# Kernel optimization log

Measured on AMD Instinct MI355X. Metric: run time of the kernel, lower is better.

The kernel has to match this reference:

```python
import jax, jax.numpy as jnp
import numpy as np

LN_EPS = 1e-6  # flax.linen.LayerNorm default


def setup_inputs() -> dict:
    key = jax.random.key(0)
    ks = jax.random.split(key, 16)
    N_TOT, M = 32768, 12            # total atoms, neighbors per atom
    ORIG, EDGE = 92, 41             # CGCNN atom / edge feature dims
    F, H, L = 128, 256, 3           # atom_fea_len, h_fea_len, n_conv

    def w(k, shape, fan_in):
        return jax.random.normal(k, shape, dtype=jnp.float32) / np.sqrt(fan_in).astype(np.float32)

    return {
        "atom_fea": jax.random.normal(ks[0], (N_TOT, ORIG), dtype=jnp.float32),
        "nbr_fea": jax.random.normal(ks[1], (N_TOT, M, EDGE), dtype=jnp.float32),
        "nbr_fea_idx": jax.random.randint(ks[2], (N_TOT, M), 0, N_TOT),
        # embedding Dense
        "W_embed": w(ks[3], (ORIG, F), ORIG), "b_embed": jnp.zeros((F,), jnp.float32),
        # per-conv-layer stacked params [L, ...]
        "W_center": w(ks[4], (L, F, F), F), "b_center": jnp.zeros((L, F), jnp.float32),
        "W_nbr": w(ks[5], (L, F, F), F), "b_nbr": jnp.zeros((L, F), jnp.float32),
        "W_edge": w(ks[6], (L, EDGE, F), EDGE), "b_edge": jnp.zeros((L, F), jnp.float32),
        "W_gate": w(ks[7], (L, F, F), F), "b_gate": jnp.zeros((L, F), jnp.float32),
        "W_mag": w(ks[8], (L, F, F), F), "b_mag": jnp.zeros((L, F), jnp.float32),
        "ln_scale": jnp.ones((L, F), jnp.float32), "ln_bias": jnp.zeros((L, F), jnp.float32),
        # readout: Dense(h) -> softplus -> Dense(1)
        "W_h": w(ks[9], (F, H), F), "b_h": jnp.zeros((H,), jnp.float32),
        "W_out": w(ks[10], (H, 1), H), "b_out": jnp.zeros((1,), jnp.float32),
        "batch_size": 128,
        "n_atoms_per_crystal": 256,
    }


def _layernorm(x, scale, bias):
    mu = jnp.mean(x, axis=-1, keepdims=True)
    var = jnp.mean(jnp.square(x - mu), axis=-1, keepdims=True)
    return (x - mu) * jax.lax.rsqrt(var + LN_EPS) * scale + bias


def reference(atom_fea, nbr_fea, nbr_fea_idx, W_embed, b_embed,
              W_center, b_center, W_nbr, b_nbr, W_edge, b_edge,
              W_gate, b_gate, W_mag, b_mag, ln_scale, ln_bias,
              W_h, b_h, W_out, b_out, batch_size, n_atoms_per_crystal):
    n_conv = W_center.shape[0]
    x = atom_fea @ W_embed + b_embed                       # [N, F]
    for i in range(n_conv):
        atom_nbr = jnp.take(x, nbr_fea_idx, axis=0)        # [N, M, F] gather
        # Dense on tiled center == Dense on center then broadcast
        phi_c = (x @ W_center[i] + b_center[i])[:, None, :]   # [N, 1, F]
        phi_n = atom_nbr @ W_nbr[i] + b_nbr[i]                # [N, M, F]
        phi_e = nbr_fea @ W_edge[i] + b_edge[i]               # [N, M, F]
        inter = phi_c * phi_n * phi_e                          # [N, M, F]
        gate = jax.nn.sigmoid(inter @ W_gate[i] + b_gate[i])
        mag = jax.nn.softplus(inter @ W_mag[i] + b_mag[i])
        nbr_sumed = jnp.sum(gate * mag, axis=1)               # [N, F]
        x = x + _layernorm(nbr_sumed, ln_scale[i], ln_bias[i])
    E_site = jax.nn.softplus(x @ W_h + b_h) @ W_out + b_out   # [N, 1]
    return jnp.sum(E_site.reshape(batch_size, n_atoms_per_crystal), axis=1, keepdims=True)  # [B, 1]
```

## Files before the change

kernel.cpp:

```cpp
#include <hip/hip_runtime.h>
#include <math.h>

#define N_TOT 32768
#define M_NBR 12
#define ORIG  92
#define EDGE  41
#define FD    128
#define HD    256
#define APC   256
#define NCRY  128

#define STR   136
#define WF_PER_LAYER 73728
#define WF_EMBED     12288
#define WF_H         32768

typedef __attribute__((ext_vector_type(8))) short bf16x8;
typedef __attribute__((ext_vector_type(4))) float f32x4;

__device__ __forceinline__ short f2bf(float f) {
    union { float f; unsigned u; } v; v.f = f;
    unsigned r = v.u + 0x7fffu + ((v.u >> 16) & 1u);
    return (short)(r >> 16);
}
__device__ __forceinline__ float bf2f(short s) {
    union { unsigned u; float f; } v; v.u = ((unsigned)(unsigned short)s) << 16;
    return v.f;
}
__device__ __forceinline__ float softplus_f(float x) {
    return fmaxf(x, 0.0f) + __logf(1.0f + __expf(-fabsf(x)));
}
__device__ __forceinline__ float sigmoid_f(float x) {
    return 1.0f / (1.0f + __expf(-x));
}

__global__ __launch_bounds__(256) void swizzle_kernel(
    const float* __restrict__ Wc_all, const float* __restrict__ Wn_all,
    const float* __restrict__ We_all, const float* __restrict__ Wg_all,
    const float* __restrict__ Wm_all, const float* __restrict__ W_embed,
    const float* __restrict__ W_h, short* __restrict__ dst_all)
{
    int gid = blockIdx.x * 256 + threadIdx.x;
    if (gid >= 33280) return;
    const float* W; short* dst; int K_real, fid, stride, l, nt, kt;
    if (gid < 27648) {
        int layer = gid / 9216;
        int rem = gid - layer * 9216;
        short* dbase = dst_all + layer * WF_PER_LAYER;
        if (rem < 2048)      { W = Wc_all + layer * 16384; dst = dbase;         K_real = 128; fid = rem; }
        else if (rem < 4096) { W = Wn_all + layer * 16384; dst = dbase + 16384; K_real = 128; fid = rem - 2048; }
        else if (rem < 5120) { W = We_all + layer * 5248;  dst = dbase + 32768; K_real = 41;  fid = rem - 4096; }
        else if (rem < 7168) { W = Wg_all + layer * 16384; dst = dbase + 40960; K_real = 128; fid = rem - 5120; }
        else                 { W = Wm_all + layer * 16384; dst = dbase + 57344; K_real = 128; fid = rem - 7168; }
        stride = 128; l = fid & 63; nt = (fid >> 6) & 7; kt = fid >> 9;
    } else if (gid < 29184) {
        fid = gid - 27648;
        W = W_embed; dst = dst_all + 3 * WF_PER_LAYER; K_real = ORIG; stride = 128;
        l = fid & 63; nt = (fid >> 6) & 7; kt = fid >> 9;
    } else {
        fid = gid - 29184;
        W = W_h; dst = dst_all + 3 * WF_PER_LAYER + WF_EMBED; K_real = 128; stride = 256;
        l = fid & 63; nt = (fid >> 6) & 15; kt = fid >> 10;
    }
    int n = nt * 16 + (l & 15), kb = kt * 32 + (l >> 4) * 8;
    bf16x8 v;
    #pragma unroll
    for (int j = 0; j < 8; ++j) {
        int k = kb + j;
        v[j] = (k < K_real) ? f2bf(W[k * stride + n]) : (short)0;
    }
    *(bf16x8*)(dst + fid * 8) = v;
}

__global__ __launch_bounds__(256) void embed_mfma_kernel(
    const float* __restrict__ atom_fea, const short* __restrict__ wef,
    const float* __restrict__ b, float* __restrict__ x, short* __restrict__ xbf)
{
    const int tid = threadIdx.x;
    const int w = tid >> 6, lane = tid & 63;
    const int q = lane >> 4, m = lane & 15;
    const int a0 = blockIdx.x * 64;
    const int arow = a0 + w * 16 + m;

    bf16x8 aA[3];
    const float* ap = atom_fea + (long)arow * ORIG;
    #pragma unroll
    for (int kt = 0; kt < 3; ++kt) {
        const int kb = kt * 32 + q * 8;
        bf16x8 v;
        if (kb + 7 < ORIG) {
            const float4 u0 = *(const float4*)(ap + kb);
            const float4 u1 = *(const float4*)(ap + kb + 4);
            v[0]=f2bf(u0.x); v[1]=f2bf(u0.y); v[2]=f2bf(u0.z); v[3]=f2bf(u0.w);
            v[4]=f2bf(u1.x); v[5]=f2bf(u1.y); v[6]=f2bf(u1.z); v[7]=f2bf(u1.w);
        } else {
            #pragma unroll
            for (int j = 0; j < 8; ++j) {
                const int k = kb + j;
                v[j] = (k < ORIG) ? f2bf(ap[k]) : (short)0;
            }
        }
        aA[kt] = v;
    }

    #pragma unroll
    for (int nt = 0; nt < 8; ++nt) {
        f32x4 C = {0.f, 0.f, 0.f, 0.f};
        #pragma unroll
        for (int kt = 0; kt < 3; ++kt)
            C = __builtin_amdgcn_mfma_f32_16x16x32_bf16(
                    aA[kt], *(const bf16x8*)(wef + ((kt * 8 + nt) * 64 + lane) * 8), C, 0, 0, 0);
        const int col = nt * 16 + m;
        const float bv = b[col];
        #pragma unroll
        for (int r = 0; r < 4; ++r) {
            const long n = a0 + w * 16 + q * 4 + r;
            const float val = C[r] + bv;
            x[n * FD + col] = val;
            xbf[n * FD + col] = f2bf(val);
        }
    }
}

__global__ __launch_bounds__(256) void conv_mfma_kernel(
    const float* __restrict__ x_in, const short* __restrict__ xbf_in,
    float* __restrict__ x_out, short* __restrict__ xbf_out,
    const float* __restrict__ nbr_fea, const int* __restrict__ nbr_idx,
    const short* __restrict__ wf,
    const float* __restrict__ bc, const float* __restrict__ bn,
    const float* __restrict__ be, const float* __restrict__ bg,
    const float* __restrict__ bm,
    const float* __restrict__ lns, const float* __restrict__ lnb)
{
    __shared__ short inter_s[192 * STR];
    __shared__ float phic_s[16 * 132];
    __shared__ int   idx_s[192];

    const int tid = threadIdx.x;
    const int w = tid >> 6, lane = tid & 63;
    const int q = lane >> 4, m = lane & 15;
    const int a0 = blockIdx.x * 16;
    const long r0 = (long)a0 * M_NBR;

    const short* Wc = wf;
    const short* Wn = wf + 16384;
    const short* We = wf + 32768;
    const short* Wg = wf + 40960;
    const short* Wm = wf + 57344;

    if (tid < 192) idx_s[tid] = nbr_idx[r0 + tid];

    {
        bf16x8 aC[4];
        #pragma unroll
        for (int kt = 0; kt < 4; ++kt)
            aC[kt] = *(const bf16x8*)(xbf_in + ((long)(a0 + m) << 7) + kt * 32 + q * 8);
        #pragma unroll
        for (int ii = 0; ii < 2; ++ii) {
            const int nt = w * 2 + ii;
            f32x4 C = {0.f, 0.f, 0.f, 0.f};
            #pragma unroll
            for (int kt = 0; kt < 4; ++kt)
                C = __builtin_amdgcn_mfma_f32_16x16x32_bf16(
                        aC[kt], *(const bf16x8*)(Wc + ((kt * 8 + nt) * 64 + lane) * 8), C, 0, 0, 0);
            const int col = nt * 16 + m;
            const float bcv = bc[col];
            #pragma unroll
            for (int r = 0; r < 4; ++r)
                phic_s[(q * 4 + r) * 132 + col] = C[r] + bcv;
        }
    }
    __syncthreads();

    bf16x8 aN[3][4];
    #pragma unroll
    for (int i = 0; i < 3; ++i) {
        const int row = (w * 3 + i) * 16 + m;
        const long g = (long)idx_s[row] << 7;
        #pragma unroll
        for (int kt = 0; kt < 4; ++kt)
            aN[i][kt] = *(const bf16x8*)(xbf_in + g + kt * 32 + q * 8);
    }
    bf16x8 aE[3][2];
    #pragma unroll
    for (int i = 0; i < 3; ++i) {
        const int row = (w * 3 + i) * 16 + m;
        const float* ep = nbr_fea + (r0 + row) * EDGE;
        bf16x8 e0, e1;
        #pragma unroll
        for (int j = 0; j < 8; ++j) e0[j] = f2bf(ep[q * 8 + j]);
        #pragma unroll
        for (int j = 0; j < 8; ++j) e1[j] = 0;
        if (q == 0) {
            #pragma unroll
            for (int j = 0; j < 8; ++j) e1[j] = f2bf(ep[32 + j]);
        } else if (q == 1) {
            e1[0] = f2bf(ep[40]);
        }
        aE[i][0] = e0; aE[i][1] = e1;
    }

    #pragma unroll
    for (int nt = 0; nt < 8; ++nt) {
        f32x4 Cn[3], Ce[3];
        #pragma unroll
        for (int i = 0; i < 3; ++i) { Cn[i] = (f32x4){0.f,0.f,0.f,0.f}; Ce[i] = (f32x4){0.f,0.f,0.f,0.f}; }
        #pragma unroll
        for (int kt = 0; kt < 4; ++kt) {
            const bf16x8 bfr = *(const bf16x8*)(Wn + ((kt * 8 + nt) * 64 + lane) * 8);
            #pragma unroll
            for (int i = 0; i < 3; ++i)
                Cn[i] = __builtin_amdgcn_mfma_f32_16x16x32_bf16(aN[i][kt], bfr, Cn[i], 0, 0, 0);
        }
        #pragma unroll
        for (int kt = 0; kt < 2; ++kt) {
            const bf16x8 efr = *(const bf16x8*)(We + ((kt * 8 + nt) * 64 + lane) * 8);
            #pragma unroll
            for (int i = 0; i < 3; ++i)
                Ce[i] = __builtin_amdgcn_mfma_f32_16x16x32_bf16(aE[i][kt], efr, Ce[i], 0, 0, 0);
        }
        const int col = nt * 16 + m;
        const float bnv = bn[col], bev = be[col];
        #pragma unroll
        for (int i = 0; i < 3; ++i) {
            const int rb = (w * 3 + i) * 16 + q * 4;
            #pragma unroll
            for (int r = 0; r < 4; ++r) {
                const int row = rb + r;
                const int atom = row / 12;
                const float iv = phic_s[atom * 132 + col] * (Cn[i][r] + bnv) * (Ce[i][r] + bev);
                inter_s[row * STR + col] = f2bf(iv);
            }
        }
    }

    bf16x8 aI[3][4];
    #pragma unroll
    for (int i = 0; i < 3; ++i) {
        const int row = (w * 3 + i) * 16 + m;
        #pragma unroll
        for (int kt = 0; kt < 4; ++kt)
            aI[i][kt] = *(const bf16x8*)(inter_s + row * STR + kt * 32 + q * 8);
    }

    #pragma unroll
    for (int nt = 0; nt < 8; ++nt) {
        f32x4 Cg[3], Cm[3];
        #pragma unroll
        for (int i = 0; i < 3; ++i) { Cg[i] = (f32x4){0.f,0.f,0.f,0.f}; Cm[i] = (f32x4){0.f,0.f,0.f,0.f}; }
        #pragma unroll
        for (int kt = 0; kt < 4; ++kt) {
            const bf16x8 gfr = *(const bf16x8*)(Wg + ((kt * 8 + nt) * 64 + lane) * 8);
            const bf16x8 mfr = *(const bf16x8*)(Wm + ((kt * 8 + nt) * 64 + lane) * 8);
            #pragma unroll
            for (int i = 0; i < 3; ++i) {
                Cg[i] = __builtin_amdgcn_mfma_f32_16x16x32_bf16(aI[i][kt], gfr, Cg[i], 0, 0, 0);
                Cm[i] = __builtin_amdgcn_mfma_f32_16x16x32_bf16(aI[i][kt], mfr, Cm[i], 0, 0, 0);
            }
        }
        const int col = nt * 16 + m;
        const float bgv = bg[col], bmv = bm[col];
        #pragma unroll
        for (int i = 0; i < 3; ++i) {
            const int rb = (w * 3 + i) * 16 + q * 4;
            #pragma unroll
            for (int r = 0; r < 4; ++r) {
                const float g = sigmoid_f(Cg[i][r] + bgv);
                const float s = softplus_f(Cm[i][r] + bmv);
                inter_s[(rb + r) * STR + col] = f2bf(g * s);
            }
        }
    }
    __syncthreads();

    {
        const int a = tid >> 4;
        const int cg = tid & 15;
        float s8[8];
        #pragma unroll
        for (int j = 0; j < 8; ++j) s8[j] = 0.f;
        #pragma unroll
        for (int nb = 0; nb < 12; ++nb) {
            const bf16x8 p = *(const bf16x8*)(inter_s + (a * 12 + nb) * STR + cg * 8);
            #pragma unroll
            for (int j = 0; j < 8; ++j) s8[j] += bf2f(p[j]);
        }
        float lsum = 0.f, lsq = 0.f;
        #pragma unroll
        for (int j = 0; j < 8; ++j) { lsum += s8[j]; lsq += s8[j] * s8[j]; }
        #pragma unroll
        for (int off = 1; off < 16; off <<= 1) {
            lsum += __shfl_xor(lsum, off, 64);
            lsq  += __shfl_xor(lsq,  off, 64);
        }
        const float mu = lsum * (1.0f / FD);
        float var = lsq * (1.0f / FD) - mu * mu;
        var = fmaxf(var, 0.0f);
        const float inv = rsqrtf(var + 1e-6f);
        const long xb = ((long)(a0 + a) << 7) + cg * 8;
        float o[8]; bf16x8 ob;
        #pragma unroll
        for (int j = 0; j < 8; ++j) {
            const int col = cg * 8 + j;
            const float y = (s8[j] - mu) * inv * lns[col] + lnb[col];
            const float v = x_in[xb + j] + y;
            o[j] = v; ob[j] = f2bf(v);
        }
        *(float4*)(x_out + xb)     = make_float4(o[0], o[1], o[2], o[3]);
        *(float4*)(x_out + xb + 4) = make_float4(o[4], o[5], o[6], o[7]);
        *(bf16x8*)(xbf_out + xb)   = ob;
    }
}

__global__ __launch_bounds__(256) void readout_mfma_kernel(
    const short* __restrict__ xbf, const short* __restrict__ whf,
    const float* __restrict__ bh, const float* __restrict__ Wo,
    const float* __restrict__ bo, float* __restrict__ out)
{
    const int tid = threadIdx.x;
    const int w = tid >> 6, lane = tid & 63;
    const int q = lane >> 4, m = lane & 15;
    const int a0 = blockIdx.x * 64;
    const int arow = a0 + w * 16 + m;

    bf16x8 aX[4];
    #pragma unroll
    for (int kt = 0; kt < 4; ++kt)
        aX[kt] = *(const bf16x8*)(xbf + ((long)arow << 7) + kt * 32 + q * 8);

    float e[4] = {0.f, 0.f, 0.f, 0.f};
    #pragma unroll
    for (int nt = 0; nt < 16; ++nt) {
        f32x4 C = {0.f, 0.f, 0.f, 0.f};
        #pragma unroll
        for (int kt = 0; kt < 4; ++kt)
            C = __builtin_amdgcn_mfma_f32_16x16x32_bf16(
                    aX[kt], *(const bf16x8*)(whf + ((kt * 16 + nt) * 64 + lane) * 8), C, 0, 0, 0);
        const int col = nt * 16 + m;
        const float bhv = bh[col], wov = Wo[col];
        #pragma unroll
        for (int r = 0; r < 4; ++r)
            e[r] += softplus_f(C[r] + bhv) * wov;
    }
    float esum = e[0] + e[1] + e[2] + e[3];
    #pragma unroll
    for (int off = 32; off > 0; off >>= 1)
        esum += __shfl_xor(esum, off, 64);
    if (lane == 0)
        atomicAdd(&out[a0 / APC], esum + 16.0f * bo[0]);
}

__global__ void zero_out_kernel(float* __restrict__ out) {
    if (threadIdx.x < NCRY) out[threadIdx.x] = 0.0f;
}

extern "C" void kernel_launch(void* const* d_in, const int* in_sizes, int n_in,
                              void* d_out, int out_size, void* d_ws, size_t ws_size,
                              hipStream_t stream) {
    const float* atom_fea = (const float*)d_in[0];
    const float* nbr_fea  = (const float*)d_in[1];
    const int*   nbr_idx  = (const int*)d_in[2];
    const float* W_embed  = (const float*)d_in[3];
    const float* b_embed  = (const float*)d_in[4];
    const float* W_center = (const float*)d_in[5];
    const float* b_center = (const float*)d_in[6];
    const float* W_nbr    = (const float*)d_in[7];
    const float* b_nbr    = (const float*)d_in[8];
    const float* W_edge   = (const float*)d_in[9];
    const float* b_edge   = (const float*)d_in[10];
    const float* W_gate   = (const float*)d_in[11];
    const float* b_gate   = (const float*)d_in[12];
    const float* W_mag    = (const float*)d_in[13];
    const float* b_mag    = (const float*)d_in[14];
    const float* ln_scale = (const float*)d_in[15];
    const float* ln_bias  = (const float*)d_in[16];
    const float* W_h      = (const float*)d_in[17];
    const float* b_h      = (const float*)d_in[18];
    const float* W_out    = (const float*)d_in[19];
    const float* b_out    = (const float*)d_in[20];

    float* out = (float*)d_out;
    const size_t NX = (size_t)N_TOT * FD;
    float* xA = (float*)d_ws;
    float* xB = xA + NX;
    short* xbfA = (short*)(xB + NX);
    short* xbfB = xbfA + NX;
    short* wfrag = xbfB + NX;

    swizzle_kernel<<<130, 256, 0, stream>>>(W_center, W_nbr, W_edge, W_gate, W_mag,
                                            W_embed, W_h, wfrag);
    embed_mfma_kernel<<<N_TOT / 64, 256, 0, stream>>>(
        atom_fea, wfrag + 3 * WF_PER_LAYER, b_embed, xA, xbfA);

    const float* xi = xA; float* xo = xB;
    const short* xbi = xbfA; short* xbo = xbfB;
    for (int l = 0; l < 3; ++l) {
        conv_mfma_kernel<<<N_TOT / 16, 256, 0, stream>>>(
            xi, xbi, xo, xbo, nbr_fea, nbr_idx,
            wfrag + (size_t)l * WF_PER_LAYER,
            b_center + (size_t)l * FD, b_nbr + (size_t)l * FD,
            b_edge + (size_t)l * FD, b_gate + (size_t)l * FD,
            b_mag + (size_t)l * FD,
            ln_scale + (size_t)l * FD, ln_bias + (size_t)l * FD);
        const float* tf = xo; xo = (float*)xi; xi = tf;
        const short* tb = xbo; xbo = (short*)xbi; xbi = tb;
    }

    zero_out_kernel<<<1, 128, 0, stream>>>(out);
    readout_mfma_kernel<<<N_TOT / 64, 256, 0, stream>>>(
        xbi, wfrag + 3 * WF_PER_LAYER + WF_EMBED, b_h, W_out, b_out, out);
}
```

Baseline: 469.3 us.

## Swap MFMA operands for row-contiguous outputs, use hardware bf16 pack and fast math

Swaps the A/B operands of the MFMA calls so each lane holds four consecutive output columns of one row. The epilogues can then use float4 bias loads and packed 64-bit stores to LDS and global memory instead of scalar strided stores. Replaces the software round-to-nearest bf16 conversion with the v_cvt_pk_bf16_f32 instruction, and uses rcp and log2 intrinsics in sigmoid and softplus to cut ALU work in the epilogues. LDS store patterns change, which may introduce bank conflicts, and the fast intrinsics slightly change numerics.

```diff
diff --git a/kernel.cpp b/kernel.cpp
--- a/kernel.cpp
+++ b/kernel.cpp
@@ -11,6 +11,7 @@
 #define NCRY  128
 
 #define STR   136
+#define PCS   132
 #define WF_PER_LAYER 73728
 #define WF_EMBED     12288
 #define WF_H         32768
@@ -18,20 +19,23 @@
 typedef __attribute__((ext_vector_type(8))) short bf16x8;
 typedef __attribute__((ext_vector_type(4))) float f32x4;
 
-__device__ __forceinline__ short f2bf(float f) {
-    union { float f; unsigned u; } v; v.f = f;
-    unsigned r = v.u + 0x7fffu + ((v.u >> 16) & 1u);
-    return (short)(r >> 16);
-}
+union BF8 { bf16x8 v; unsigned u[4]; };
+
+__device__ __forceinline__ unsigned pk2(float lo, float hi) {
+    unsigned r;
+    asm("v_cvt_pk_bf16_f32 %0, %1, %2" : "=v"(r) : "v"(lo), "v"(hi));
+    return r;
+}
+__device__ __forceinline__ short f2bf(float f) { return (short)pk2(f, f); }
 __device__ __forceinline__ float bf2f(short s) {
     union { unsigned u; float f; } v; v.u = ((unsigned)(unsigned short)s) << 16;
     return v.f;
 }
 __device__ __forceinline__ float softplus_f(float x) {
-    return fmaxf(x, 0.0f) + __logf(1.0f + __expf(-fabsf(x)));
+    return fmaxf(x, 0.0f) + 0.6931471805599453f * __log2f(1.0f + __expf(-fabsf(x)));
 }
 __device__ __forceinline__ float sigmoid_f(float x) {
-    return 1.0f / (1.0f + __expf(-x));
+    return __builtin_amdgcn_rcpf(1.0f + __expf(-x));
 }
 
 __global__ __launch_bounds__(256) void swizzle_kernel(
@@ -82,43 +86,37 @@
     const int a0 = blockIdx.x * 64;
     const int arow = a0 + w * 16 + m;
 
-    bf16x8 aA[3];
+    BF8 aA[3];
     const float* ap = atom_fea + (long)arow * ORIG;
     #pragma unroll
     for (int kt = 0; kt < 3; ++kt) {
         const int kb = kt * 32 + q * 8;
-        bf16x8 v;
+        BF8 t;
         if (kb + 7 < ORIG) {
             const float4 u0 = *(const float4*)(ap + kb);
             const float4 u1 = *(const float4*)(ap + kb + 4);
-            v[0]=f2bf(u0.x); v[1]=f2bf(u0.y); v[2]=f2bf(u0.z); v[3]=f2bf(u0.w);
-            v[4]=f2bf(u1.x); v[5]=f2bf(u1.y); v[6]=f2bf(u1.z); v[7]=f2bf(u1.w);
+            t.u[0] = pk2(u0.x, u0.y); t.u[1] = pk2(u0.z, u0.w);
+            t.u[2] = pk2(u1.x, u1.y); t.u[3] = pk2(u1.z, u1.w);
         } else {
-            #pragma unroll
-            for (int j = 0; j < 8; ++j) {
-                const int k = kb + j;
-                v[j] = (k < ORIG) ? f2bf(ap[k]) : (short)0;
-            }
-        }
-        aA[kt] = v;
-    }
-
-    #pragma unroll
-    for (int nt = 0; nt < 8; ++nt) {
+            const float4 u0 = *(const float4*)(ap + kb);
+            t.u[0] = pk2(u0.x, u0.y); t.u[1] = pk2(u0.z, u0.w);
+            t.u[2] = 0u; t.u[3] = 0u;
+        }
+        aA[kt] = t;
+    }
+
+    #pragma unroll
+    for (int ct = 0; ct < 8; ++ct) {
         f32x4 C = {0.f, 0.f, 0.f, 0.f};
         #pragma unroll
         for (int kt = 0; kt < 3; ++kt)
             C = __builtin_amdgcn_mfma_f32_16x16x32_bf16(
-                    aA[kt], *(const bf16x8*)(wef + ((kt * 8 + nt) * 64 + lane) * 8), C, 0, 0, 0);
-        const int col = nt * 16 + m;
-        const float bv = b[col];
-        #pragma unroll
-        for (int r = 0; r < 4; ++r) {
-            const long n = a0 + w * 16 + q * 4 + r;
-            const float val = C[r] + bv;
-            x[n * FD + col] = val;
-            xbf[n * FD + col] = f2bf(val);
-        }
+                    *(const bf16x8*)(wef + ((kt * 8 + ct) * 64 + lane) * 8), aA[kt].v, C, 0, 0, 0);
+        const float4 bv = *(const float4*)(b + ct * 16 + q * 4);
+        const float o0 = C[0] + bv.x, o1 = C[1] + bv.y, o2 = C[2] + bv.z, o3 = C[3] + bv.w;
+        const long base = ((long)arow << 7) + ct * 16 + q * 4;
+        *(float4*)(x + base) = make_float4(o0, o1, o2, o3);
+        *(uint2*)(xbf + base) = make_uint2(pk2(o0, o1), pk2(o2, o3));
     }
 }
 
@@ -133,7 +131,7 @@
     const float* __restrict__ lns, const float* __restrict__ lnb)
 {
     __shared__ short inter_s[192 * STR];
-    __shared__ float phic_s[16 * 132];
+    __shared__ float phic_s[16 * PCS];
     __shared__ int   idx_s[192];
 
     const int tid = threadIdx.x;
@@ -157,17 +155,15 @@
             aC[kt] = *(const bf16x8*)(xbf_in + ((long)(a0 + m) << 7) + kt * 32 + q * 8);
         #pragma unroll
         for (int ii = 0; ii < 2; ++ii) {
-            const int nt = w * 2 + ii;
+            const int ct = w * 2 + ii;
             f32x4 C = {0.f, 0.f, 0.f, 0.f};
             #pragma unroll
             for (int kt = 0; kt < 4; ++kt)
                 C = __builtin_amdgcn_mfma_f32_16x16x32_bf16(
-                        aC[kt], *(const bf16x8*)(Wc + ((kt * 8 + nt) * 64 + lane) * 8), C, 0, 0, 0);
-            const int col = nt * 16 + m;
-            const float bcv = bc[col];
-            #pragma unroll
-            for (int r = 0; r < 4; ++r)
-                phic_s[(q * 4 + r) * 132 + col] = C[r] + bcv;
+                        *(const bf16x8*)(Wc + ((kt * 8 + ct) * 64 + lane) * 8), aC[kt], C, 0, 0, 0);
+            const float4 bv = *(const float4*)(bc + ct * 16 + q * 4);
+            *(float4*)(phic_s + m * PCS + ct * 16 + q * 4) =
+                make_float4(C[0] + bv.x, C[1] + bv.y, C[2] + bv.z, C[3] + bv.w);
         }
     }
     __syncthreads();
@@ -186,51 +182,62 @@
     for (int i = 0; i < 3; ++i) {
         const int row = (w * 3 + i) * 16 + m;
         const float* ep = nbr_fea + (r0 + row) * EDGE;
-        bf16x8 e0, e1;
-        #pragma unroll
-        for (int j = 0; j < 8; ++j) e0[j] = f2bf(ep[q * 8 + j]);
-        #pragma unroll
-        for (int j = 0; j < 8; ++j) e1[j] = 0;
+        BF8 e0, e1;
+        const int kb = q * 8;
+        e0.u[0] = pk2(ep[kb + 0], ep[kb + 1]);
+        e0.u[1] = pk2(ep[kb + 2], ep[kb + 3]);
+        e0.u[2] = pk2(ep[kb + 4], ep[kb + 5]);
+        e0.u[3] = pk2(ep[kb + 6], ep[kb + 7]);
+        e1.u[0] = 0u; e1.u[1] = 0u; e1.u[2] = 0u; e1.u[3] = 0u;
         if (q == 0) {
-            #pragma unroll
-            for (int j = 0; j < 8; ++j) e1[j] = f2bf(ep[32 + j]);
+            e1.u[0] = pk2(ep[32], ep[33]);
+            e1.u[1] = pk2(ep[34], ep[35]);
+            e1.u[2] = pk2(ep[36], ep[37]);
+            e1.u[3] = pk2(ep[38], ep[39]);
         } else if (q == 1) {
-            e1[0] = f2bf(ep[40]);
-        }
-        aE[i][0] = e0; aE[i][1] = e1;
-    }
-
-    #pragma unroll
-    for (int nt = 0; nt < 8; ++nt) {
+            e1.u[0] = pk2(ep[40], 0.0f);
+        }
+        aE[i][0] = e0.v; aE[i][1] = e1.v;
+    }
+
+    int atomL[3];
+    #pragma unroll
+    for (int i = 0; i < 3; ++i)
+        atomL[i] = (w * 48 + i * 16 + m) / 12;
+
+    #pragma unroll
+    for (int ct = 0; ct < 8; ++ct) {
         f32x4 Cn[3], Ce[3];
         #pragma unroll
-        for (int i = 0; i < 3; ++i) { Cn[i] = (f32x4){0.f,0.f,0.f,0.f}; Ce[i] = (f32x4){0.f,0.f,0.f,0.f}; }
+        for (int i = 0; i < 3; ++i) {
+            Cn[i] = (f32x4){0.f, 0.f, 0.f, 0.f};
+            Ce[i] = (f32x4){0.f, 0.f, 0.f, 0.f};
+        }
         #pragma unroll
         for (int kt = 0; kt < 4; ++kt) {
-            const bf16x8 bfr = *(const bf16x8*)(Wn + ((kt * 8 + nt) * 64 + lane) * 8);
+            const bf16x8 nfr = *(const bf16x8*)(Wn + ((kt * 8 + ct) * 64 + lane) * 8);
             #pragma unroll
             for (int i = 0; i < 3; ++i)
-                Cn[i] = __builtin_amdgcn_mfma_f32_16x16x32_bf16(aN[i][kt], bfr, Cn[i], 0, 0, 0);
+                Cn[i] = __builtin_amdgcn_mfma_f32_16x16x32_bf16(nfr, aN[i][kt], Cn[i], 0, 0, 0);
         }
         #pragma unroll
         for (int kt = 0; kt < 2; ++kt) {
-            const bf16x8 efr = *(const bf16x8*)(We + ((kt * 8 + nt) * 64 + lane) * 8);
+            const bf16x8 efr = *(const bf16x8*)(We + ((kt * 8 + ct) * 64 + lane) * 8);
             #pragma unroll
             for (int i = 0; i < 3; ++i)
-                Ce[i] = __builtin_amdgcn_mfma_f32_16x16x32_bf16(aE[i][kt], efr, Ce[i], 0, 0, 0);
-        }
-        const int col = nt * 16 + m;
-        const float bnv = bn[col], bev = be[col];
+                Ce[i] = __builtin_amdgcn_mfma_f32_16x16x32_bf16(efr, aE[i][kt], Ce[i], 0, 0, 0);
+        }
+        const float4 bnv = *(const float4*)(bn + ct * 16 + q * 4);
+        const float4 bev = *(const float4*)(be + ct * 16 + q * 4);
         #pragma unroll
         for (int i = 0; i < 3; ++i) {
-            const int rb = (w * 3 + i) * 16 + q * 4;
-            #pragma unroll
-            for (int r = 0; r < 4; ++r) {
-                const int row = rb + r;
-                const int atom = row / 12;
-                const float iv = phic_s[atom * 132 + col] * (Cn[i][r] + bnv) * (Ce[i][r] + bev);
-                inter_s[row * STR + col] = f2bf(iv);
-            }
+            const float4 pc = *(const float4*)(phic_s + atomL[i] * PCS + ct * 16 + q * 4);
+            const float v0 = pc.x * (Cn[i][0] + bnv.x) * (Ce[i][0] + bev.x);
+            const float v1 = pc.y * (Cn[i][1] + bnv.y) * (Ce[i][1] + bev.y);
+            const float v2 = pc.z * (Cn[i][2] + bnv.z) * (Ce[i][2] + bev.z);
+            const float v3 = pc.w * (Cn[i][3] + bnv.w) * (Ce[i][3] + bev.w);
+            *(uint2*)(inter_s + (w * 48 + i * 16 + m) * STR + ct * 16 + q * 4) =
+                make_uint2(pk2(v0, v1), pk2(v2, v3));
         }
     }
 
@@ -244,31 +251,33 @@
     }
 
     #pragma unroll
-    for (int nt = 0; nt < 8; ++nt) {
+    for (int ct = 0; ct < 8; ++ct) {
         f32x4 Cg[3], Cm[3];
         #pragma unroll
-        for (int i = 0; i < 3; ++i) { Cg[i] = (f32x4){0.f,0.f,0.f,0.f}; Cm[i] = (f32x4){0.f,0.f,0.f,0.f}; }
+        for (int i = 0; i < 3; ++i) {
+            Cg[i] = (f32x4){0.f, 0.f, 0.f, 0.f};
+            Cm[i] = (f32x4){0.f, 0.f, 0.f, 0.f};
+        }
         #pragma unroll
         for (int kt = 0; kt < 4; ++kt) {
-            const bf16x8 gfr = *(const bf16x8*)(Wg + ((kt * 8 + nt) * 64 + lane) * 8);
-            const bf16x8 mfr = *(const bf16x8*)(Wm + ((kt * 8 + nt) * 64 + lane) * 8);
+            const bf16x8 gfr = *(const bf16x8*)(Wg + ((kt * 8 + ct) * 64 + lane) * 8);
+            const bf16x8 mfr = *(const bf16x8*)(Wm + ((kt * 8 + ct) * 64 + lane) * 8);
             #pragma unroll
             for (int i = 0; i < 3; ++i) {
-                Cg[i] = __builtin_amdgcn_mfma_f32_16x16x32_bf16(aI[i][kt], gfr, Cg[i], 0, 0, 0);
-                Cm[i] = __builtin_amdgcn_mfma_f32_16x16x32_bf16(aI[i][kt], mfr, Cm[i], 0, 0, 0);
+                Cg[i] = __builtin_amdgcn_mfma_f32_16x16x32_bf16(gfr, aI[i][kt], Cg[i], 0, 0, 0);
+                Cm[i] = __builtin_amdgcn_mfma_f32_16x16x32_bf16(mfr, aI[i][kt], Cm[i], 0, 0, 0);
             }
         }
-        const int col = nt * 16 + m;
-        const float bgv = bg[col], bmv = bm[col];
+        const float4 bgv = *(const float4*)(bg + ct * 16 + q * 4);
+        const float4 bmv = *(const float4*)(bm + ct * 16 + q * 4);
         #pragma unroll
         for (int i = 0; i < 3; ++i) {
-            const int rb = (w * 3 + i) * 16 + q * 4;
-            #pragma unroll
-            for (int r = 0; r < 4; ++r) {
-                const float g = sigmoid_f(Cg[i][r] + bgv);
-                const float s = softplus_f(Cm[i][r] + bmv);
-                inter_s[(rb + r) * STR + col] = f2bf(g * s);
-            }
+            const float v0 = sigmoid_f(Cg[i][0] + bgv.x) * softplus_f(Cm[i][0] + bmv.x);
+            const float v1 = sigmoid_f(Cg[i][1] + bgv.y) * softplus_f(Cm[i][1] + bmv.y);
+            const float v2 = sigmoid_f(Cg[i][2] + bgv.z) * softplus_f(Cm[i][2] + bmv.z);
+            const float v3 = sigmoid_f(Cg[i][3] + bgv.w) * softplus_f(Cm[i][3] + bmv.w);
+            *(uint2*)(inter_s + (w * 48 + i * 16 + m) * STR + ct * 16 + q * 4) =
+                make_uint2(pk2(v0, v1), pk2(v2, v3));
         }
     }
     __syncthreads();
@@ -298,17 +307,25 @@
         var = fmaxf(var, 0.0f);
         const float inv = rsqrtf(var + 1e-6f);
         const long xb = ((long)(a0 + a) << 7) + cg * 8;
-        float o[8]; bf16x8 ob;
-        #pragma unroll
-        for (int j = 0; j < 8; ++j) {
-            const int col = cg * 8 + j;
-            const float y = (s8[j] - mu) * inv * lns[col] + lnb[col];
-            const float v = x_in[xb + j] + y;
-            o[j] = v; ob[j] = f2bf(v);
-        }
+        float xv[8], sc[4], sc2[4], bb[4], bb2[4];
+        *(float4*)&xv[0] = *(const float4*)(x_in + xb);
+        *(float4*)&xv[4] = *(const float4*)(x_in + xb + 4);
+        *(float4*)&sc[0]  = *(const float4*)(lns + cg * 8);
+        *(float4*)&sc2[0] = *(const float4*)(lns + cg * 8 + 4);
+        *(float4*)&bb[0]  = *(const float4*)(lnb + cg * 8);
+        *(float4*)&bb2[0] = *(const float4*)(lnb + cg * 8 + 4);
+        float o[8];
+        #pragma unroll
+        for (int j = 0; j < 4; ++j) {
+            o[j]     = xv[j]     + (s8[j]     - mu) * inv * sc[j]  + bb[j];
+            o[j + 4] = xv[j + 4] + (s8[j + 4] - mu) * inv * sc2[j] + bb2[j];
+        }
+        BF8 ob;
+        ob.u[0] = pk2(o[0], o[1]); ob.u[1] = pk2(o[2], o[3]);
+        ob.u[2] = pk2(o[4], o[5]); ob.u[3] = pk2(o[6], o[7]);
         *(float4*)(x_out + xb)     = make_float4(o[0], o[1], o[2], o[3]);
         *(float4*)(x_out + xb + 4) = make_float4(o[4], o[5], o[6], o[7]);
-        *(bf16x8*)(xbf_out + xb)   = ob;
+        *(bf16x8*)(xbf_out + xb)   = ob.v;
     }
 }
 
```

Measured after the change: 410.7 us. 1.14x faster.
